# Performance work log

Measured on AMD Instinct MI355X. Metric: run time of the kernel, lower is better.

The kernel has to match this reference:

```python
import jax, jax.numpy as jnp
import numpy as np

TAU = 2.0
THR = 0.5
ALPHA = 4.0  # Sigmoid_Grad surrogate sharpness
EPS = 1e-5
HEADS = 16
SCALE = 0.25

@jax.custom_vjp
def spike(v):
    return (v > 0.0).astype(v.dtype)

def _spike_fwd(v):
    return (v > 0.0).astype(v.dtype), v

def _spike_bwd(v, g):
    s = jax.nn.sigmoid(ALPHA * v)
    return (g * ALPHA * s * (1.0 - s),)

spike.defvjp(_spike_fwd, _spike_bwd)

def lif(x):
    # x: (T, ...) ; stateful LIF over leading time dim, hard reset (detached spike)
    def step(mem, xt):
        mem = mem + (xt - mem) / TAU
        s = spike(mem - THR)
        mem = mem * (1.0 - jax.lax.stop_gradient(s))
        return mem, s
    _, s = jax.lax.scan(step, jnp.zeros_like(x[0]), x)
    return s

def bn(x, p):
    # x: (T,B,C,N), p: (4,C) = (gamma, beta, mean, var); inference-form BatchNorm1d
    g, b, m, v = p
    shp = (1, 1, -1, 1)
    return (x - m.reshape(shp)) * (g.reshape(shp) / jnp.sqrt(v.reshape(shp) + EPS)) + b.reshape(shp)

def conv_bn_lif(x, w, p, bias=None):
    # 1x1 Conv1d == channel matmul: (T,B,Cin,N) x (Cout,Cin) -> (T,B,Cout,N)
    y = jnp.einsum('tbcn,oc->tbon', x, w)
    if bias is not None:
        y = y + bias.reshape(1, 1, -1, 1)
    return lif(bn(y, p))

def _block(x, q_w, q_bn, k_w, k_bn, v_w, v_bn, proj_w, proj_bn,
           fc1_w, fc1_b, fc1_bn, fc2_w, fc2_b, fc2_bn):
    T, B, C, N = x.shape
    D = C // HEADS

    def to_heads(y):  # (T,B,C,N) -> (T,B,H,N,D)
        return y.transpose(0, 1, 3, 2).reshape(T, B, N, HEADS, D).transpose(0, 1, 3, 2, 4)

    q = to_heads(conv_bn_lif(x, q_w, q_bn))
    k = to_heads(conv_bn_lif(x, k_w, k_bn))
    v = to_heads(conv_bn_lif(x, v_w, v_bn))

    attn = jnp.einsum('tbhnd,tbhmd->tbhnm', q, k) * SCALE  # no softmax
    r = jnp.einsum('tbhnm,tbhmd->tbhnd', attn, v) * SCALE
    r = r.transpose(0, 1, 2, 4, 3).reshape(T, B, C, N)  # (T,B,H,D,N) -> (T,B,C,N)
    r = lif(r)  # attn_lif
    attn_out = conv_bn_lif(r, proj_w, proj_bn)  # proj conv+bn+lif

    x = x + attn_out  # residual 1

    h = conv_bn_lif(x, fc1_w, fc1_bn, fc1_b)
    m = conv_bn_lif(h, fc2_w, fc2_bn, fc2_b)
    return x + m  # residual 2

def setup_inputs() -> dict:
    key = jax.random.key(0)
    ks = jax.random.split(key, 16)
    T, B, C, N = 4, 16, 256, 512
    H = 1024  # mlp hidden = 4*C
    w = 0.05
    d = {}
    d['x'] = jax.random.normal(ks[0], (T, B, C, N), jnp.float32)
    d['q_w'] = jax.random.normal(ks[1], (C, C), jnp.float32) * w
    d['q_bn'] = jax.random.uniform(ks[2], (4, C), jnp.float32, 0.5, 1.5)
    d['k_w'] = jax.random.normal(ks[3], (C, C), jnp.float32) * w
    d['k_bn'] = jax.random.uniform(ks[4], (4, C), jnp.float32, 0.5, 1.5)
    d['v_w'] = jax.random.normal(ks[5], (C, C), jnp.float32) * w
    d['v_bn'] = jax.random.uniform(ks[6], (4, C), jnp.float32, 0.5, 1.5)
    d['proj_w'] = jax.random.normal(ks[7], (C, C), jnp.float32) * w
    d['proj_bn'] = jax.random.uniform(ks[8], (4, C), jnp.float32, 0.5, 1.5)
    d['fc1_w'] = jax.random.normal(ks[9], (H, C), jnp.float32) * w
    d['fc1_b'] = jnp.zeros((H,), jnp.float32)
    d['fc1_bn'] = jax.random.uniform(ks[10], (4, H), jnp.float32, 0.5, 1.5)
    d['fc2_w'] = jax.random.normal(ks[11], (C, H), jnp.float32) * w
    d['fc2_b'] = jnp.zeros((C,), jnp.float32)
    d['fc2_bn'] = jax.random.uniform(ks[12], (4, C), jnp.float32, 0.5, 1.5)
    return d

def reference(x, q_w, q_bn, k_w, k_bn, v_w, v_bn, proj_w, proj_bn,
              fc1_w, fc1_b, fc1_bn, fc2_w, fc2_b, fc2_bn):
    return _block(x, q_w, q_bn, k_w, k_bn, v_w, v_bn, proj_w, proj_bn,
                  fc1_w, fc1_b, fc1_bn, fc2_w, fc2_b, fc2_bn)
```

## Files before the change

### kernel.cpp

```cpp
#include <hip/hip_runtime.h>

#pragma clang fp contract(off)

typedef unsigned char u8;
typedef unsigned int u32;

#define TSTEPS 4

template <int XMODE, bool HASX2, int OMODE>
__global__ __launch_bounds__(256) void conv_bn_lif(
    const void* __restrict__ X1v, const u8* __restrict__ X2,
    const float* __restrict__ Wt, const float* __restrict__ bias,
    const float* __restrict__ bnp,
    u8* __restrict__ Sout,
    const float* __restrict__ Xres, const u8* __restrict__ AOres,
    float* __restrict__ Fout,
    int Bsz, int Cin, int Cout, int N)
{
  const int tid = threadIdx.x;
  const int tx = tid & 15, ty = tid >> 4;
  const int nBase = blockIdx.x * 64, oBase = blockIdx.y * 64, b = blockIdx.z;
  const int KT = Cin >> 5;
  const int TT = TSTEPS * KT;

  __shared__ __align__(16) float Xs[2][32][68];
  __shared__ __align__(16) float Ws[2][32][68];

  float sc[4], mn[4], bt[4], bi[4];
  #pragma unroll
  for (int i = 0; i < 4; ++i) {
    int o = oBase + ty * 4 + i;
    float g  = bnp[0 * Cout + o];
    float be = bnp[1 * Cout + o];
    float m  = bnp[2 * Cout + o];
    float vv = bnp[3 * Cout + o];
    float d_f = (float)((double)vv + (double)1e-5f);
    float s_f = (float)sqrt((double)d_f);
    sc[i] = (float)((double)g / (double)s_f);
    mn[i] = m; bt[i] = be;
    bi[i] = bias ? bias[o] : 0.0f;
  }

  float mem[4][4], acc[4][4];
  #pragma unroll
  for (int i = 0; i < 4; ++i)
    #pragma unroll
    for (int j = 0; j < 4; ++j) { mem[i][j] = 0.0f; acc[i][j] = 0.0f; }

  const int xRow = tid >> 3;
  const int xC8  = (tid & 7) * 8;
  const int wO   = tid >> 2;
  const int wK8  = (tid & 3) * 8;

  float4 pxa, pxb, pwa, pwb;
  uint2 pxu, pau;

  auto issue = [&](int i) {
    const int tI = i / KT, k0 = (i % KT) << 5;
    const size_t xb = (size_t)(tI * Bsz + b) * Cin * N
                    + (size_t)(k0 + xRow) * N + nBase + xC8;
    if constexpr (XMODE == 0) {
      pxa = *(const float4*)((const float*)X1v + xb);
      pxb = *(const float4*)((const float*)X1v + xb + 4);
    } else {
      pxu = *(const uint2*)((const u8*)X1v + xb);
    }
    if constexpr (HASX2) pau = *(const uint2*)(X2 + xb);
    const size_t wb = (size_t)(oBase + wO) * Cin + k0 + wK8;
    pwa = *(const float4*)(Wt + wb);
    pwb = *(const float4*)(Wt + wb + 4);
  };

  auto commit = [&](int buf) {
    float xv[8];
    if constexpr (XMODE == 0) {
      xv[0] = pxa.x; xv[1] = pxa.y; xv[2] = pxa.z; xv[3] = pxa.w;
      xv[4] = pxb.x; xv[5] = pxb.y; xv[6] = pxb.z; xv[7] = pxb.w;
    } else {
      #pragma unroll
      for (int j = 0; j < 4; ++j) xv[j]     = (float)((pxu.x >> (8 * j)) & 0xffu);
      #pragma unroll
      for (int j = 0; j < 4; ++j) xv[4 + j] = (float)((pxu.y >> (8 * j)) & 0xffu);
    }
    if constexpr (HASX2) {
      #pragma unroll
      for (int j = 0; j < 4; ++j) xv[j]     = xv[j]     + (float)((pau.x >> (8 * j)) & 0xffu);
      #pragma unroll
      for (int j = 0; j < 4; ++j) xv[4 + j] = xv[4 + j] + (float)((pau.y >> (8 * j)) & 0xffu);
    }
    *(float4*)&Xs[buf][xRow][xC8]     = make_float4(xv[0], xv[1], xv[2], xv[3]);
    *(float4*)&Xs[buf][xRow][xC8 + 4] = make_float4(xv[4], xv[5], xv[6], xv[7]);
    Ws[buf][wK8 + 0][wO] = pwa.x;  Ws[buf][wK8 + 1][wO] = pwa.y;
    Ws[buf][wK8 + 2][wO] = pwa.z;  Ws[buf][wK8 + 3][wO] = pwa.w;
    Ws[buf][wK8 + 4][wO] = pwb.x;  Ws[buf][wK8 + 5][wO] = pwb.y;
    Ws[buf][wK8 + 6][wO] = pwb.z;  Ws[buf][wK8 + 7][wO] = pwb.w;
  };

  issue(0);
  commit(0);
  __syncthreads();

  for (int tt = 0; tt < TT; ++tt) {
    const int buf = tt & 1;
    if (tt + 1 < TT) issue(tt + 1);

    #pragma unroll
    for (int kk = 0; kk < 32; ++kk) {
      float4 wv = *(const float4*)&Ws[buf][kk][ty * 4];
      float4 xv = *(const float4*)&Xs[buf][kk][tx * 4];
      float wa[4] = {wv.x, wv.y, wv.z, wv.w};
      float xa[4] = {xv.x, xv.y, xv.z, xv.w};
      #pragma unroll
      for (int i = 0; i < 4; ++i)
        #pragma unroll
        for (int j = 0; j < 4; ++j)
          acc[i][j] = fmaf(wa[i], xa[j], acc[i][j]);
    }

    if ((tt % KT) == KT - 1) {
      const int t = tt / KT;
      const size_t sbase = (size_t)(t * Bsz + b) * Cout * N;
      #pragma unroll
      for (int i = 0; i < 4; ++i) {
        const size_t rb = sbase + (size_t)(oBase + ty * 4 + i) * N + nBase + tx * 4;
        if constexpr (OMODE == 0) {
          u32 pack = 0;
          #pragma unroll
          for (int j = 0; j < 4; ++j) {
            float y = acc[i][j];
            if (bias) y = y + bi[i];
            float t1 = y - mn[i];
            float t2 = t1 * sc[i];
            y = t2 + bt[i];
            float m2 = mem[i][j];
            float dd = y - m2;
            m2 = m2 + dd * 0.5f;
            bool sp = (m2 - 0.5f) > 0.0f;
            mem[i][j] = sp ? 0.0f : m2;
            if (sp) pack |= (1u << (8 * j));
            acc[i][j] = 0.0f;
          }
          *(u32*)&Sout[rb] = pack;
        } else {
          float4 xr = *(const float4*)&Xres[rb];
          u32 av = *(const u32*)&AOres[rb];
          float xa4[4] = {xr.x, xr.y, xr.z, xr.w};
          float o4[4];
          #pragma unroll
          for (int j = 0; j < 4; ++j) {
            float y = acc[i][j];
            if (bias) y = y + bi[i];
            float t1 = y - mn[i];
            float t2 = t1 * sc[i];
            y = t2 + bt[i];
            float m2 = mem[i][j];
            float dd = y - m2;
            m2 = m2 + dd * 0.5f;
            bool sp = (m2 - 0.5f) > 0.0f;
            mem[i][j] = sp ? 0.0f : m2;
            float s = sp ? 1.0f : 0.0f;
            float xn = xa4[j] + (float)((av >> (8 * j)) & 0xffu);
            o4[j] = xn + s;
            acc[i][j] = 0.0f;
          }
          *(float4*)&Fout[rb] = make_float4(o4[0], o4[1], o4[2], o4[3]);
        }
      }
    }

    __syncthreads();
    if (tt + 1 < TT) commit((tt + 1) & 1);
    __syncthreads();
  }
}

__global__ __launch_bounds__(256) void attn_lif(
    const u8* __restrict__ Qs, const u8* __restrict__ Ks,
    const u8* __restrict__ Vs, u8* __restrict__ Rs,
    int Bsz, int C, int N)
{
  const int tid = threadIdx.x;
  const int h = blockIdx.x & 15;
  const int b = blockIdx.x >> 4;

  __shared__ u8 qs[16][528];
  __shared__ u8 ks[16][528];
  __shared__ u8 vs[16][528];
  __shared__ int Gs[16][17];

  const int eG = tid >> 4;
  const int dG = tid & 15;
  const int dR = tid >> 4;
  const int nR0 = tid & 15;

  float mem[32];
  #pragma unroll
  for (int i = 0; i < 32; ++i) mem[i] = 0.0f;

  for (int t = 0; t < TSTEPS; ++t) {
    __syncthreads();
    const size_t base = ((size_t)(t * Bsz + b) * C + h * 16) * N;
    for (int i = 0; i < 32; ++i) {
      int flat = tid + 256 * i;
      int d = flat >> 9, n = flat & 511;
      size_t g = base + (size_t)d * N + n;
      qs[d][n] = Qs[g];
      ks[d][n] = Ks[g];
      vs[d][n] = Vs[g];
    }
    __syncthreads();

    int gi = 0;
    for (int n = 0; n < 512; ++n)
      gi += (int)ks[eG][n] * (int)vs[dG][n];
    Gs[eG][dG] = gi;
    __syncthreads();

    int Greg[16];
    #pragma unroll
    for (int e = 0; e < 16; ++e) Greg[e] = Gs[e][dR];

    const size_t obase = ((size_t)(t * Bsz + b) * C + h * 16 + dR) * N;
    for (int j = 0; j < 32; ++j) {
      int n = nR0 + 16 * j;
      int ri = 0;
      #pragma unroll
      for (int e = 0; e < 16; ++e)
        ri += qs[e][n] ? Greg[e] : 0;
      float r = (float)ri * 0.0625f;
      float m2 = mem[j];
      float d = r - m2;
      m2 = m2 + d * 0.5f;
      float s = (m2 - 0.5f) > 0.0f ? 1.0f : 0.0f;
      mem[j] = (s > 0.0f) ? 0.0f : m2;
      Rs[obase + n] = (s > 0.0f) ? (u8)1 : (u8)0;
    }
  }
}

extern "C" void kernel_launch(void* const* d_in, const int* in_sizes, int n_in,
                              void* d_out, int out_size, void* d_ws, size_t ws_size,
                              hipStream_t stream)
{
  const float* x     = (const float*)d_in[0];
  const float* q_w   = (const float*)d_in[1];
  const float* q_bn  = (const float*)d_in[2];
  const float* k_w   = (const float*)d_in[3];
  const float* k_bn  = (const float*)d_in[4];
  const float* v_w   = (const float*)d_in[5];
  const float* v_bn  = (const float*)d_in[6];
  const float* p_w   = (const float*)d_in[7];
  const float* p_bn  = (const float*)d_in[8];
  const float* f1_w  = (const float*)d_in[9];
  const float* f1_b  = (const float*)d_in[10];
  const float* f1_bn = (const float*)d_in[11];
  const float* f2_w  = (const float*)d_in[12];
  const float* f2_b  = (const float*)d_in[13];
  const float* f2_bn = (const float*)d_in[14];

  const int T = 4, B = 16, C = 256, N = 512, Hm = 1024;
  const size_t SZ = (size_t)T * B * C * N;

  char* ws = (char*)d_ws;
  u8* q_s  = (u8*)(ws + 0 * SZ);
  u8* k_s  = (u8*)(ws + 1 * SZ);
  u8* v_s  = (u8*)(ws + 2 * SZ);
  u8* r_s  = (u8*)(ws + 3 * SZ);
  u8* ao_s = (u8*)(ws + 4 * SZ);
  u8* h_s  = (u8*)(ws + 0 * SZ);

  dim3 blk(256);
  dim3 gC(N / 64, C / 64, B);

  conv_bn_lif<0, false, 0><<<gC, blk, 0, stream>>>(
      x, nullptr, q_w, nullptr, q_bn, q_s, nullptr, nullptr, nullptr, B, C, C, N);
  conv_bn_lif<0, false, 0><<<gC, blk, 0, stream>>>(
      x, nullptr, k_w, nullptr, k_bn, k_s, nullptr, nullptr, nullptr, B, C, C, N);
  conv_bn_lif<0, false, 0><<<gC, blk, 0, stream>>>(
      x, nullptr, v_w, nullptr, v_bn, v_s, nullptr, nullptr, nullptr, B, C, C, N);
  attn_lif<<<dim3(B * 16), blk, 0, stream>>>(q_s, k_s, v_s, r_s, B, C, N);
  conv_bn_lif<1, false, 0><<<gC, blk, 0, stream>>>(
      r_s, nullptr, p_w, nullptr, p_bn, ao_s, nullptr, nullptr, nullptr, B, C, C, N);
  conv_bn_lif<0, true, 0><<<dim3(N / 64, Hm / 64, B), blk, 0, stream>>>(
      x, ao_s, f1_w, f1_b, f1_bn, h_s, nullptr, nullptr, nullptr, B, C, Hm, N);
  conv_bn_lif<1, false, 1><<<gC, blk, 0, stream>>>(
      h_s, nullptr, f2_w, f2_b, f2_bn, nullptr, x, ao_s, (float*)d_out, B, Hm, C, N);
}
```

Baseline: 984.9 us.

## Fuse QKV convs, enlarge register tiles, and bit-pack spike inputs in shared memory

The three Q/K/V conv launches become one kernel that reads each X tile once and computes three weight groups with wider N tiles (8 columns per thread). fc1 computes four 64-row output groups per block, so the X+ao input tile is reused four times. Spike (u8) inputs to proj and fc2 are packed into bitmasks in shared memory, and the weight rows get padding to spread LDS bank accesses. The cost is many more registers per thread (launch_bounds 256,1) and fewer blocks in the grid, which lowers occupancy.

```diff
diff --git a/kernel.cpp b/kernel.cpp
--- a/kernel.cpp
+++ b/kernel.cpp
@@ -7,93 +7,132 @@
 
 #define TSTEPS 4
 
-template <int XMODE, bool HASX2, int OMODE>
-__global__ __launch_bounds__(256) void conv_bn_lif(
-    const void* __restrict__ X1v, const u8* __restrict__ X2,
-    const float* __restrict__ Wt, const float* __restrict__ bias,
-    const float* __restrict__ bnp,
-    u8* __restrict__ Sout,
-    const float* __restrict__ Xres, const u8* __restrict__ AOres,
-    float* __restrict__ Fout,
-    int Bsz, int Cin, int Cout, int N)
+__device__ __forceinline__ constexpr int wrow(int k) {
+  return k * 68 + (k >> 3) * 16;
+}
+
+struct ConvArgs {
+  const void* X1;
+  const u8* X2;
+  const float* W[4];
+  const float* bn[4];
+  const float* bias[4];
+  u8* out[4];
+  const float* Xres;
+  const u8* AOres;
+  float* Fout;
+  int oAdd[4];
+  int Bsz, Cin, CoutTot, N, OB;
+};
+
+template <int G, int J, int XM, int OM>
+__global__ __launch_bounds__(256, 1) void conv_bn_lif(ConvArgs a)
 {
   const int tid = threadIdx.x;
   const int tx = tid & 15, ty = tid >> 4;
-  const int nBase = blockIdx.x * 64, oBase = blockIdx.y * 64, b = blockIdx.z;
-  const int KT = Cin >> 5;
-  const int TT = TSTEPS * KT;
-
-  __shared__ __align__(16) float Xs[2][32][68];
-  __shared__ __align__(16) float Ws[2][32][68];
-
-  float sc[4], mn[4], bt[4], bi[4];
+  const int nBase = blockIdx.x * (J * 16);
+  const int by = blockIdx.y, b = blockIdx.z;
+  const int KT = a.Cin >> 5, TT = TSTEPS * KT;
+  constexpr int XP  = J * 16 + 4;
+  constexpr int XSZ = (XM == 2) ? 64 : 32 * XP;
+  constexpr int NW  = J / 2;
+
+  __shared__ float XsF[2][XSZ];
+  __shared__ float WsF[G][2][2224];
+
+  float sc[G][4], mn[G][4], bt[G][4], bi[G][4];
   #pragma unroll
-  for (int i = 0; i < 4; ++i) {
-    int o = oBase + ty * 4 + i;
-    float g  = bnp[0 * Cout + o];
-    float be = bnp[1 * Cout + o];
-    float m  = bnp[2 * Cout + o];
-    float vv = bnp[3 * Cout + o];
-    float d_f = (float)((double)vv + (double)1e-5f);
-    float s_f = (float)sqrt((double)d_f);
-    sc[i] = (float)((double)g / (double)s_f);
-    mn[i] = m; bt[i] = be;
-    bi[i] = bias ? bias[o] : 0.0f;
-  }
-
-  float mem[4][4], acc[4][4];
+  for (int g = 0; g < G; ++g) {
+    #pragma unroll
+    for (int i = 0; i < 4; ++i) {
+      int o = by * a.OB + a.oAdd[g] + ty * 4 + i;
+      float gg = a.bn[g][0 * a.CoutTot + o];
+      float be = a.bn[g][1 * a.CoutTot + o];
+      float m  = a.bn[g][2 * a.CoutTot + o];
+      float vv = a.bn[g][3 * a.CoutTot + o];
+      float d_f = (float)((double)vv + (double)1e-5f);
+      float s_f = (float)sqrt((double)d_f);
+      sc[g][i] = (float)((double)gg / (double)s_f);
+      mn[g][i] = m; bt[g][i] = be;
+      bi[g][i] = a.bias[g] ? a.bias[g][o] : 0.0f;
+    }
+  }
+
+  float acc[G][4][J], mem[G][4][J];
   #pragma unroll
-  for (int i = 0; i < 4; ++i)
-    #pragma unroll
-    for (int j = 0; j < 4; ++j) { mem[i][j] = 0.0f; acc[i][j] = 0.0f; }
+  for (int g = 0; g < G; ++g)
+    #pragma unroll
+    for (int i = 0; i < 4; ++i)
+      #pragma unroll
+      for (int j = 0; j < J; ++j) { acc[g][i][j] = 0.0f; mem[g][i][j] = 0.0f; }
 
   const int xRow = tid >> 3;
-  const int xC8  = (tid & 7) * 8;
+  const int xCs  = (tid & 7) * 4;
+  const int bKb  = tid >> 6;
+  const int bN   = tid & 63;
   const int wO   = tid >> 2;
   const int wK8  = (tid & 3) * 8;
-
-  float4 pxa, pxb, pwa, pwb;
-  uint2 pxu, pau;
+  const int wBase = wK8 * 68 + (tid & 3) * 16 + wO;
+
+  float4 px[NW]; u32 pa[NW]; u32 pb8[8];
+  float4 pw[G][2];
 
   auto issue = [&](int i) {
     const int tI = i / KT, k0 = (i % KT) << 5;
-    const size_t xb = (size_t)(tI * Bsz + b) * Cin * N
-                    + (size_t)(k0 + xRow) * N + nBase + xC8;
-    if constexpr (XMODE == 0) {
-      pxa = *(const float4*)((const float*)X1v + xb);
-      pxb = *(const float4*)((const float*)X1v + xb + 4);
+    if constexpr (XM == 2) {
+      const u8* xp = (const u8*)a.X1 +
+          (size_t)(tI * a.Bsz + b) * a.Cin * a.N +
+          (size_t)(k0 + bKb * 8) * a.N + nBase + bN;
+      #pragma unroll
+      for (int j = 0; j < 8; ++j) pb8[j] = xp[(size_t)j * a.N];
     } else {
-      pxu = *(const uint2*)((const u8*)X1v + xb);
-    }
-    if constexpr (HASX2) pau = *(const uint2*)(X2 + xb);
-    const size_t wb = (size_t)(oBase + wO) * Cin + k0 + wK8;
-    pwa = *(const float4*)(Wt + wb);
-    pwb = *(const float4*)(Wt + wb + 4);
+      const size_t xb0 = (size_t)(tI * a.Bsz + b) * a.Cin * a.N +
+                         (size_t)(k0 + xRow) * a.N + nBase + xCs;
+      #pragma unroll
+      for (int jj = 0; jj < NW; ++jj) {
+        px[jj] = *(const float4*)((const float*)a.X1 + xb0 + 32 * jj);
+        if constexpr (XM == 1) pa[jj] = *(const u32*)(a.X2 + xb0 + 32 * jj);
+      }
+    }
+    #pragma unroll
+    for (int g = 0; g < G; ++g) {
+      const float* wr = a.W[g] +
+          (size_t)(by * a.OB + a.oAdd[g] + wO) * a.Cin + k0 + wK8;
+      pw[g][0] = *(const float4*)wr;
+      pw[g][1] = *(const float4*)(wr + 4);
+    }
   };
 
   auto commit = [&](int buf) {
-    float xv[8];
-    if constexpr (XMODE == 0) {
-      xv[0] = pxa.x; xv[1] = pxa.y; xv[2] = pxa.z; xv[3] = pxa.w;
-      xv[4] = pxb.x; xv[5] = pxb.y; xv[6] = pxb.z; xv[7] = pxb.w;
+    if constexpr (XM == 2) {
+      u32 v = 0;
+      #pragma unroll
+      for (int j = 0; j < 8; ++j) v |= (pb8[j] & 1u) << j;
+      ((u8*)XsF[buf])[bN * 4 + bKb] = (u8)v;
     } else {
-      #pragma unroll
-      for (int j = 0; j < 4; ++j) xv[j]     = (float)((pxu.x >> (8 * j)) & 0xffu);
-      #pragma unroll
-      for (int j = 0; j < 4; ++j) xv[4 + j] = (float)((pxu.y >> (8 * j)) & 0xffu);
-    }
-    if constexpr (HASX2) {
-      #pragma unroll
-      for (int j = 0; j < 4; ++j) xv[j]     = xv[j]     + (float)((pau.x >> (8 * j)) & 0xffu);
-      #pragma unroll
-      for (int j = 0; j < 4; ++j) xv[4 + j] = xv[4 + j] + (float)((pau.y >> (8 * j)) & 0xffu);
-    }
-    *(float4*)&Xs[buf][xRow][xC8]     = make_float4(xv[0], xv[1], xv[2], xv[3]);
-    *(float4*)&Xs[buf][xRow][xC8 + 4] = make_float4(xv[4], xv[5], xv[6], xv[7]);
-    Ws[buf][wK8 + 0][wO] = pwa.x;  Ws[buf][wK8 + 1][wO] = pwa.y;
-    Ws[buf][wK8 + 2][wO] = pwa.z;  Ws[buf][wK8 + 3][wO] = pwa.w;
-    Ws[buf][wK8 + 4][wO] = pwb.x;  Ws[buf][wK8 + 5][wO] = pwb.y;
-    Ws[buf][wK8 + 6][wO] = pwb.z;  Ws[buf][wK8 + 7][wO] = pwb.w;
+      float* xd = &XsF[buf][xRow * XP + xCs];
+      #pragma unroll
+      for (int jj = 0; jj < NW; ++jj) {
+        float4 v = px[jj];
+        if constexpr (XM == 1) {
+          u32 av = pa[jj];
+          v.x = v.x + (float)(av & 0xffu);
+          v.y = v.y + (float)((av >> 8) & 0xffu);
+          v.z = v.z + (float)((av >> 16) & 0xffu);
+          v.w = v.w + (float)((av >> 24) & 0xffu);
+        }
+        *(float4*)(xd + 32 * jj) = v;
+      }
+    }
+    #pragma unroll
+    for (int g = 0; g < G; ++g) {
+      float* wd = WsF[g][buf];
+      #pragma unroll
+      for (int i = 0; i < 4; ++i) {
+        wd[wBase + (i + 0) * 68] = (&pw[g][0].x)[i];
+        wd[wBase + (i + 4) * 68] = (&pw[g][1].x)[i];
+      }
+    }
   };
 
   issue(0);
@@ -104,66 +143,92 @@
     const int buf = tt & 1;
     if (tt + 1 < TT) issue(tt + 1);
 
+    uint4 xw;
+    if constexpr (XM == 2)
+      xw = *(const uint4*)((const u32*)XsF[buf] + tx * 4);
+
     #pragma unroll
     for (int kk = 0; kk < 32; ++kk) {
-      float4 wv = *(const float4*)&Ws[buf][kk][ty * 4];
-      float4 xv = *(const float4*)&Xs[buf][kk][tx * 4];
-      float wa[4] = {wv.x, wv.y, wv.z, wv.w};
-      float xa[4] = {xv.x, xv.y, xv.z, xv.w};
-      #pragma unroll
-      for (int i = 0; i < 4; ++i)
+      float xa[J];
+      if constexpr (XM == 2) {
+        xa[0] = (float)((xw.x >> kk) & 1u);
+        xa[1] = (float)((xw.y >> kk) & 1u);
+        xa[2] = (float)((xw.z >> kk) & 1u);
+        xa[3] = (float)((xw.w >> kk) & 1u);
+      } else {
+        float4 v0 = *(const float4*)&XsF[buf][kk * XP + tx * 4];
+        xa[0] = v0.x; xa[1] = v0.y; xa[2] = v0.z; xa[3] = v0.w;
+        if constexpr (J == 8) {
+          float4 v1 = *(const float4*)&XsF[buf][kk * XP + tx * 4 + 64];
+          xa[4] = v1.x; xa[5] = v1.y; xa[6] = v1.z; xa[7] = v1.w;
+        }
+      }
+      #pragma unroll
+      for (int g = 0; g < G; ++g) {
+        float4 wv = *(const float4*)&WsF[g][buf][wrow(kk) + ty * 4];
+        float wa[4] = {wv.x, wv.y, wv.z, wv.w};
         #pragma unroll
-        for (int j = 0; j < 4; ++j)
-          acc[i][j] = fmaf(wa[i], xa[j], acc[i][j]);
+        for (int i = 0; i < 4; ++i)
+          #pragma unroll
+          for (int j = 0; j < J; ++j)
+            acc[g][i][j] = fmaf(wa[i], xa[j], acc[g][i][j]);
+      }
     }
 
     if ((tt % KT) == KT - 1) {
       const int t = tt / KT;
-      const size_t sbase = (size_t)(t * Bsz + b) * Cout * N;
-      #pragma unroll
-      for (int i = 0; i < 4; ++i) {
-        const size_t rb = sbase + (size_t)(oBase + ty * 4 + i) * N + nBase + tx * 4;
-        if constexpr (OMODE == 0) {
-          u32 pack = 0;
+      #pragma unroll
+      for (int g = 0; g < G; ++g) {
+        #pragma unroll
+        for (int i = 0; i < 4; ++i) {
+          const int og = by * a.OB + a.oAdd[g] + ty * 4 + i;
           #pragma unroll
-          for (int j = 0; j < 4; ++j) {
-            float y = acc[i][j];
-            if (bias) y = y + bi[i];
-            float t1 = y - mn[i];
-            float t2 = t1 * sc[i];
-            y = t2 + bt[i];
-            float m2 = mem[i][j];
-            float dd = y - m2;
-            m2 = m2 + dd * 0.5f;
-            bool sp = (m2 - 0.5f) > 0.0f;
-            mem[i][j] = sp ? 0.0f : m2;
-            if (sp) pack |= (1u << (8 * j));
-            acc[i][j] = 0.0f;
+          for (int s = 0; s < J / 4; ++s) {
+            const size_t rb = ((size_t)(t * a.Bsz + b) * a.CoutTot + og) * a.N
+                            + nBase + tx * 4 + 64 * s;
+            if constexpr (OM == 0) {
+              u32 pack = 0;
+              #pragma unroll
+              for (int j = 0; j < 4; ++j) {
+                const int jj = s * 4 + j;
+                float y = acc[g][i][jj] + bi[g][i];
+                float t1 = y - mn[g][i];
+                float t2 = t1 * sc[g][i];
+                y = t2 + bt[g][i];
+                float m2 = mem[g][i][jj];
+                float dd = y - m2;
+                m2 = m2 + dd * 0.5f;
+                bool sp = (m2 - 0.5f) > 0.0f;
+                mem[g][i][jj] = sp ? 0.0f : m2;
+                if (sp) pack |= (1u << (8 * j));
+                acc[g][i][jj] = 0.0f;
+              }
+              *(u32*)&a.out[g][rb] = pack;
+            } else {
+              float4 xr = *(const float4*)&a.Xres[rb];
+              u32 av = *(const u32*)&a.AOres[rb];
+              float xa4[4] = {xr.x, xr.y, xr.z, xr.w};
+              float o4[4];
+              #pragma unroll
+              for (int j = 0; j < 4; ++j) {
+                const int jj = s * 4 + j;
+                float y = acc[g][i][jj] + bi[g][i];
+                float t1 = y - mn[g][i];
+                float t2 = t1 * sc[g][i];
+                y = t2 + bt[g][i];
+                float m2 = mem[g][i][jj];
+                float dd = y - m2;
+                m2 = m2 + dd * 0.5f;
+                bool sp = (m2 - 0.5f) > 0.0f;
+                mem[g][i][jj] = sp ? 0.0f : m2;
+                float sv = sp ? 1.0f : 0.0f;
+                float xn = xa4[j] + (float)((av >> (8 * j)) & 0xffu);
+                o4[j] = xn + sv;
+                acc[g][i][jj] = 0.0f;
+              }
+              *(float4*)&a.Fout[rb] = make_float4(o4[0], o4[1], o4[2], o4[3]);
+            }
           }
-          *(u32*)&Sout[rb] = pack;
-        } else {
-          float4 xr = *(const float4*)&Xres[rb];
-          u32 av = *(const u32*)&AOres[rb];
-          float xa4[4] = {xr.x, xr.y, xr.z, xr.w};
-          float o4[4];
-          #pragma unroll
-          for (int j = 0; j < 4; ++j) {
-            float y = acc[i][j];
-            if (bias) y = y + bi[i];
-            float t1 = y - mn[i];
-            float t2 = t1 * sc[i];
-            y = t2 + bt[i];
-            float m2 = mem[i][j];
-            float dd = y - m2;
-            m2 = m2 + dd * 0.5f;
-            bool sp = (m2 - 0.5f) > 0.0f;
-            mem[i][j] = sp ? 0.0f : m2;
-            float s = sp ? 1.0f : 0.0f;
-            float xn = xa4[j] + (float)((av >> (8 * j)) & 0xffu);
-            o4[j] = xn + s;
-            acc[i][j] = 0.0f;
-          }
-          *(float4*)&Fout[rb] = make_float4(o4[0], o4[1], o4[2], o4[3]);
         }
       }
     }
@@ -188,10 +253,8 @@
   __shared__ u8 vs[16][528];
   __shared__ int Gs[16][17];
 
-  const int eG = tid >> 4;
-  const int dG = tid & 15;
-  const int dR = tid >> 4;
-  const int nR0 = tid & 15;
+  const int eG = tid >> 4, dG = tid & 15;
+  const int dR = tid >> 4, nR0 = tid & 15;
 
   float mem[32];
   #pragma unroll
@@ -270,19 +333,44 @@
   u8* h_s  = (u8*)(ws + 0 * SZ);
 
   dim3 blk(256);
-  dim3 gC(N / 64, C / 64, B);
-
-  conv_bn_lif<0, false, 0><<<gC, blk, 0, stream>>>(
-      x, nullptr, q_w, nullptr, q_bn, q_s, nullptr, nullptr, nullptr, B, C, C, N);
-  conv_bn_lif<0, false, 0><<<gC, blk, 0, stream>>>(
-      x, nullptr, k_w, nullptr, k_bn, k_s, nullptr, nullptr, nullptr, B, C, C, N);
-  conv_bn_lif<0, false, 0><<<gC, blk, 0, stream>>>(
-      x, nullptr, v_w, nullptr, v_bn, v_s, nullptr, nullptr, nullptr, B, C, C, N);
+
+  {
+    ConvArgs a = {};
+    a.X1 = x;
+    a.W[0] = q_w; a.W[1] = k_w; a.W[2] = v_w;
+    a.bn[0] = q_bn; a.bn[1] = k_bn; a.bn[2] = v_bn;
+    a.out[0] = q_s; a.out[1] = k_s; a.out[2] = v_s;
+    a.Bsz = B; a.Cin = C; a.CoutTot = C; a.N = N; a.OB = 64;
+    conv_bn_lif<3, 8, 0, 0><<<dim3(N / 128, C / 64, B), blk, 0, stream>>>(a);
+  }
+
   attn_lif<<<dim3(B * 16), blk, 0, stream>>>(q_s, k_s, v_s, r_s, B, C, N);
-  conv_bn_lif<1, false, 0><<<gC, blk, 0, stream>>>(
-      r_s, nullptr, p_w, nullptr, p_bn, ao_s, nullptr, nullptr, nullptr, B, C, C, N);
-  conv_bn_lif<0, true, 0><<<dim3(N / 64, Hm / 64, B), blk, 0, stream>>>(
-      x, ao_s, f1_w, f1_b, f1_bn, h_s, nullptr, nullptr, nullptr, B, C, Hm, N);
-  conv_bn_lif<1, false, 1><<<gC, blk, 0, stream>>>(
-      h_s, nullptr, f2_w, f2_b, f2_bn, nullptr, x, ao_s, (float*)d_out, B, Hm, C, N);
+
+  {
+    ConvArgs a = {};
+    a.X1 = r_s;
+    a.W[0] = p_w; a.bn[0] = p_bn; a.out[0] = ao_s;
+    a.Bsz = B; a.Cin = C; a.CoutTot = C; a.N = N; a.OB = 64;
+    conv_bn_lif<1, 4, 2, 0><<<dim3(N / 64, C / 64, B), blk, 0, stream>>>(a);
+  }
+
+  {
+    ConvArgs a = {};
+    a.X1 = x; a.X2 = ao_s;
+    for (int g = 0; g < 4; ++g) {
+      a.W[g] = f1_w; a.bn[g] = f1_bn; a.bias[g] = f1_b; a.out[g] = h_s;
+      a.oAdd[g] = g * 64;
+    }
+    a.Bsz = B; a.Cin = C; a.CoutTot = Hm; a.N = N; a.OB = 256;
+    conv_bn_lif<4, 8, 1, 0><<<dim3(N / 128, Hm / 256, B), blk, 0, stream>>>(a);
+  }
+
+  {
+    ConvArgs a = {};
+    a.X1 = h_s;
+    a.W[0] = f2_w; a.bn[0] = f2_bn; a.bias[0] = f2_b;
+    a.Xres = x; a.AOres = ao_s; a.Fout = (float*)d_out;
+    a.Bsz = B; a.Cin = Hm; a.CoutTot = C; a.N = N; a.OB = 64;
+    conv_bn_lif<1, 4, 2, 1><<<dim3(N / 64, C / 64, B), blk, 0, stream>>>(a);
+  }
 }
```

Measured after the change: 1.183 ms. +20.1%, slower.
